# Optimization experiments

Measured on AMD Instinct MI355X. Metric: run time of the kernel, lower is better.

Reference implementation:

```python
import jax, jax.numpy as jnp
import numpy as np

D = 4  # downsample factor

def _conv1x1(x, w, b):
    # x: [B,C,H,W], w: [O,C], b: [O]
    return jnp.einsum('bchw,oc->bohw', x, w) + b[None, :, None, None]

def _maxpool(y):
    B, c, h, w = y.shape
    return y.reshape(B, c, h // D, D, w // D, D).max(axis=(3, 5))

def setup_inputs() -> dict:
    key = jax.random.key(0)
    ks = jax.random.split(key, 8)
    B, C, H, W = 4, 128, 256, 256
    cqk = C // 8
    s = 0.05
    return {
        'x':  jax.random.normal(ks[0], (B, C, H, W), jnp.float32),
        'wq': jax.random.normal(ks[1], (cqk, C), jnp.float32) * s,
        'bq': jnp.zeros((cqk,), jnp.float32),
        'wk': jax.random.normal(ks[2], (cqk, C), jnp.float32) * s,
        'bk': jnp.zeros((cqk,), jnp.float32),
        'wv': jax.random.normal(ks[3], (C, C), jnp.float32) * s,
        'bv': jnp.zeros((C,), jnp.float32),
        'gamma': jnp.zeros((1,), jnp.float32),
    }

def reference(x, wq, bq, wk, bk, wv, bv, gamma):
    B, C, H, W = x.shape
    N = (H // D) * (W // D)
    q = _maxpool(_conv1x1(x, wq, bq)).reshape(B, -1, N).transpose(0, 2, 1)  # [B,N,c]
    k = _maxpool(_conv1x1(x, wk, bk)).reshape(B, -1, N)                     # [B,c,N]
    energy = jnp.einsum('bnc,bcm->bnm', q, k)                               # [B,N,N]
    attention = jax.nn.softmax(energy, axis=-1)
    v = _maxpool(_conv1x1(x, wv, bv)).reshape(B, C, N)                      # [B,C,N]
    # torch: matmul(v, attention^T) -> out[b,c,m] = sum_n v[b,c,n] * attn[b,m,n]
    out = jnp.einsum('bcn,bmn->bcm', v, attention)
    out = out.reshape(B, C, H // D, W // D)
    out = jnp.repeat(jnp.repeat(out, D, axis=2), D, axis=3)  # nearest upsample
    out = gamma * out + x
    return out, attention
```

## Files before the change

### kernel.cpp

```cpp
#include <hip/hip_runtime.h>

#define B_ 4
#define C_ 128
#define H_ 256
#define W_ 256
#define CQK 16
#define NPOOL 4096
#define KSPLIT 2

typedef short bf16x8 __attribute__((ext_vector_type(8)));
typedef float f32x4 __attribute__((ext_vector_type(4)));
typedef float f32x2 __attribute__((ext_vector_type(2)));
typedef unsigned short ushort8 __attribute__((ext_vector_type(8)));

__device__ __forceinline__ unsigned short f2bf(float f) {
    unsigned int u = __float_as_uint(f);
    unsigned int r = (u + 0x7fffu + ((u >> 16) & 1u)) >> 16;
    return (unsigned short)r;
}

__global__ __launch_bounds__(256) void qk_conv_k(
    const float* __restrict__ x,
    const float* __restrict__ wq, const float* __restrict__ bq,
    const float* __restrict__ wk, const float* __restrict__ bk,
    const float* __restrict__ gamma,
    float* __restrict__ qpT, float* __restrict__ kp,
    float* __restrict__ out)
{
    if (gamma[0] != 0.0f) return;

    const int wh = blockIdx.x;
    const int ph = blockIdx.y;
    const int b  = blockIdx.z;
    const int t  = threadIdx.x;
    const int hl = t >> 6;
    const int ln = t & 63;

    __shared__ float wlds[C_ * 36];
    __shared__ float red[4 * 32 * 33];

    #pragma unroll
    for (int q = 0; q < 16; ++q) {
        const int idx = q*256 + t;
        const int c = idx & 127, o = idx >> 7;
        wlds[c*36 + o] = (o < 16) ? wq[o*C_ + c] : wk[(o-16)*C_ + c];
    }
    __syncthreads();

    float acc[32][2];
    #pragma unroll
    for (int o = 0; o < 32; ++o) { acc[o][0] = 0.f; acc[o][1] = 0.f; }

    const size_t base = ((size_t)(b*C_)*H_ + ph*4 + hl)*W_ + wh*128 + ln*2;
    const f32x2* xp = (const f32x2*)(x + base);
    f32x2*       op = (f32x2*)(out + base);

    f32x2 pre[4];
    #pragma unroll
    for (int q = 0; q < 4; ++q) pre[q] = xp[(size_t)q * 32768];

    #pragma unroll 4
    for (int c = 0; c < C_; ++c) {
        const f32x2 xv = pre[c & 3];
        if (c + 4 < C_) pre[c & 3] = xp[(size_t)(c + 4) * 32768];
        __builtin_nontemporal_store(xv, &op[(size_t)c * 32768]);
        const float* wrow = &wlds[c*36];
        #pragma unroll
        for (int og = 0; og < 8; ++og) {
            const f32x4 w4 = *(const f32x4*)&wrow[og*4];
            #pragma unroll
            for (int j = 0; j < 4; ++j) {
                acc[og*4+j][0] = fmaf(w4[j], xv[0], acc[og*4+j][0]);
                acc[og*4+j][1] = fmaf(w4[j], xv[1], acc[og*4+j][1]);
            }
        }
    }

    #pragma unroll
    for (int o = 0; o < 32; ++o) {
        float mm = fmaxf(acc[o][0], acc[o][1]);
        mm = fmaxf(mm, __shfl_xor(mm, 1));
        if (!(ln & 1)) red[(hl*32 + (ln >> 1))*33 + o] = mm;
    }
    __syncthreads();

    const int n0 = ph*64 + wh*32;
    #pragma unroll
    for (int q = 0; q < 4; ++q) {
        const int p = q*256 + t;
        const int o = p & 31, j = p >> 5;
        float val = fmaxf(fmaxf(red[(0*32+j)*33+o], red[(1*32+j)*33+o]),
                          fmaxf(red[(2*32+j)*33+o], red[(3*32+j)*33+o]));
        const int n = n0 + j;
        if (o < 16) { val += bq[o];    qpT[((size_t)b*NPOOL + n)*CQK + o] = val; }
        else        { val += bk[o-16]; kp[(b*CQK + (o-16))*NPOOL + n] = val; }
    }
}

__global__ __launch_bounds__(256) void qkv_pool_k(
    const float* __restrict__ x,
    const float* __restrict__ wq, const float* __restrict__ bq,
    const float* __restrict__ wk, const float* __restrict__ bk,
    const float* __restrict__ wv, const float* __restrict__ bv,
    const float* __restrict__ gamma,
    float* __restrict__ qpT, float* __restrict__ kp,
    unsigned short* __restrict__ vbf)
{
    if (gamma[0] == 0.0f) return;

    const int og = blockIdx.x;
    const int qw = blockIdx.y;
    const int b  = blockIdx.z >> 6;
    const int ph = blockIdx.z & 63;
    const int t  = threadIdx.x;
    const int o0 = og * 32;

    __shared__ float xs[32][256];
    __shared__ float wst[32][36];
    __shared__ float red[2][16][33];

    const int oq    = t & 7;
    const int tp    = t >> 3;
    const int hl_lo = tp >> 4;
    const int w4    = tp & 15;

    float acc[2][4][4];
    #pragma unroll
    for (int a = 0; a < 2; ++a)
        #pragma unroll
        for (int j = 0; j < 4; ++j)
            #pragma unroll
            for (int k = 0; k < 4; ++k) acc[a][j][k] = 0.f;

    const int hb = t >> 6;
    const int wb = t & 63;

    for (int c0 = 0; c0 < C_; c0 += 32) {
        __syncthreads();
        #pragma unroll 4
        for (int cl = 0; cl < 32; ++cl) {
            xs[cl][t] = x[((size_t)((b*C_ + c0 + cl)*H_ + ph*4 + hb))*W_ + qw*64 + wb];
        }
        {
            const int idx = t * 4;
            const int cl  = idx >> 5;
            const int olb = idx & 31;
            #pragma unroll
            for (int j = 0; j < 4; ++j) {
                const int ol = olb + j;
                const int o  = o0 + ol;
                const int c  = c0 + cl;
                float wv_;
                if (o < 16)      wv_ = wq[o*C_ + c];
                else if (o < 32) wv_ = wk[(o-16)*C_ + c];
                else             wv_ = wv[(o-32)*C_ + c];
                wst[cl][ol] = wv_;
            }
        }
        __syncthreads();
        for (int cl = 0; cl < 32; ++cl) {
            const float4 wv4 = *(const float4*)&wst[cl][oq*4];
            const float4 xa  = *(const float4*)&xs[cl][hl_lo*64 + w4*4];
            const float4 xb  = *(const float4*)&xs[cl][(2+hl_lo)*64 + w4*4];
            const float wr[4]  = {wv4.x, wv4.y, wv4.z, wv4.w};
            const float xar[4] = {xa.x, xa.y, xa.z, xa.w};
            const float xbr[4] = {xb.x, xb.y, xb.z, xb.w};
            #pragma unroll
            for (int j = 0; j < 4; ++j)
                #pragma unroll
                for (int k = 0; k < 4; ++k) {
                    acc[0][j][k] = fmaf(wr[j], xar[k], acc[0][j][k]);
                    acc[1][j][k] = fmaf(wr[j], xbr[k], acc[1][j][k]);
                }
        }
    }

    float m[4];
    #pragma unroll
    for (int j = 0; j < 4; ++j) {
        float mm = acc[0][j][0];
        #pragma unroll
        for (int k = 0; k < 4; ++k) {
            mm = fmaxf(mm, acc[0][j][k]);
            mm = fmaxf(mm, acc[1][j][k]);
        }
        m[j] = mm;
    }
    __syncthreads();
    #pragma unroll
    for (int j = 0; j < 4; ++j) red[hl_lo][w4][oq*4 + j] = m[j];
    __syncthreads();

    const int n0 = ph*64 + qw*16;
    #pragma unroll
    for (int r = 0; r < 2; ++r) {
        const int ii = t + r*256;
        const int pw = ii & 15, o = ii >> 4;
        float val = fmaxf(red[0][pw][o], red[1][pw][o]);
        const int n = n0 + pw;
        if (og == 0) {
            if (o < 16) { val += bq[o];    qpT[((size_t)b*NPOOL + n)*CQK + o] = val; }
            else        { val += bk[o-16]; kp[(b*CQK + (o-16))*NPOOL + n] = val; }
        } else {
            const int c = o0 - 32 + o;
            val += bv[c];
            vbf[(size_t)(b*C_ + c)*NPOOL + n] = f2bf(val);
        }
    }
}

__global__ __launch_bounds__(256) void attn_k(
    const float* __restrict__ qpT, const float* __restrict__ kp,
    float* __restrict__ attn)
{
    const int bid = blockIdx.x;
    const int b  = bid >> 10;
    const int i0 = (bid & 1023) * 4;
    const int t  = threadIdx.x;

    __shared__ float qs[4][16];
    __shared__ float wredm[4][4];
    __shared__ float wreds[4][4];

    if (t < 64) {
        const int i = t >> 4, c = t & 15;
        qs[i][c] = qpT[((size_t)b*NPOOL + i0 + i)*CQK + c];
    }
    __syncthreads();

    float acc[4][16];
    #pragma unroll
    for (int i = 0; i < 4; ++i)
        #pragma unroll
        for (int j = 0; j < 16; ++j) acc[i][j] = 0.f;

    const f32x4* k4 = (const f32x4*)kp;
    for (int c = 0; c < CQK; ++c) {
        float qr[4];
        #pragma unroll
        for (int i = 0; i < 4; ++i) qr[i] = qs[i][c];
        #pragma unroll
        for (int u = 0; u < 4; ++u) {
            const f32x4 kv = k4[(((size_t)(b*CQK + c))*NPOOL >> 2) + u*256 + t];
            #pragma unroll
            for (int i = 0; i < 4; ++i)
                #pragma unroll
                for (int e = 0; e < 4; ++e)
                    acc[i][u*4+e] = fmaf(qr[i], kv[e], acc[i][u*4+e]);
        }
    }

    const int wid = t >> 6, lane = t & 63;

    float rmax[4];
    #pragma unroll
    for (int i = 0; i < 4; ++i) {
        float lm = acc[i][0];
        #pragma unroll
        for (int j = 1; j < 16; ++j) lm = fmaxf(lm, acc[i][j]);
        #pragma unroll
        for (int off = 32; off; off >>= 1) lm = fmaxf(lm, __shfl_xor(lm, off));
        if (lane == 0) wredm[i][wid] = lm;
    }
    __syncthreads();
    #pragma unroll
    for (int i = 0; i < 4; ++i)
        rmax[i] = fmaxf(fmaxf(wredm[i][0], wredm[i][1]), fmaxf(wredm[i][2], wredm[i][3]));

    #pragma unroll
    for (int i = 0; i < 4; ++i) {
        float ls = 0.f;
        #pragma unroll
        for (int j = 0; j < 16; ++j) { acc[i][j] = __expf(acc[i][j] - rmax[i]); ls += acc[i][j]; }
        #pragma unroll
        for (int off = 32; off; off >>= 1) ls += __shfl_xor(ls, off);
        if (lane == 0) wreds[i][wid] = ls;
    }
    __syncthreads();
    f32x4* a4 = (f32x4*)attn;
    #pragma unroll
    for (int i = 0; i < 4; ++i) {
        const float s   = wreds[i][0] + wreds[i][1] + wreds[i][2] + wreds[i][3];
        const float inv = 1.0f / s;
        const size_t base = ((size_t)(b*NPOOL + i0 + i) * NPOOL) >> 2;
        #pragma unroll
        for (int u = 0; u < 4; ++u) {
            f32x4 r;
            r[0] = acc[i][u*4+0]*inv; r[1] = acc[i][u*4+1]*inv;
            r[2] = acc[i][u*4+2]*inv; r[3] = acc[i][u*4+3]*inv;
            __builtin_nontemporal_store(r, &a4[base + u*256 + t]);
        }
    }
}

__global__ __launch_bounds__(256) void pv_mfma_k(
    const unsigned short* __restrict__ vb, const float* __restrict__ attn,
    const float* __restrict__ gamma, float* __restrict__ os)
{
    if (gamma[0] == 0.0f) return;

    const int it = blockIdx.x;
    const int b  = blockIdx.y;
    const int z  = blockIdx.z;
    const int i0 = it * 128;
    const int t  = threadIdx.x;
    const int lane = t & 63, wid = t >> 6;
    const int wm = wid >> 1, wn = wid & 1;
    const int lr = lane & 15, lg = lane >> 4;

    __shared__ unsigned short As[128 * 72];
    __shared__ unsigned short Bs[128 * 72];

    f32x4 acc[4][4];
    #pragma unroll
    for (int m = 0; m < 4; ++m)
        #pragma unroll
        for (int n = 0; n < 4; ++n)
            acc[m][n] = (f32x4){0.f, 0.f, 0.f, 0.f};

    const int rowA = t >> 3;
    const int cb   = (t & 7) * 8;

    ushort8 ra[4];
    float4  rb[4][2];

    auto load_tile = [&](int nn) {
        #pragma unroll
        for (int p = 0; p < 4; ++p) {
            const int r = p * 32 + rowA;
            ra[p] = *(const ushort8*)&vb[(size_t)(b*C_ + r)*NPOOL + nn + cb];
            const float* src = &attn[(size_t)(b*NPOOL + i0 + r)*NPOOL + nn + cb];
            rb[p][0] = *(const float4*)src;
            rb[p][1] = *(const float4*)(src + 4);
        }
    };

    int nn = z * (NPOOL / KSPLIT);
    load_tile(nn);

    for (int s = 0; s < (NPOOL / KSPLIT) / 64; ++s) {
        __syncthreads();
        #pragma unroll
        for (int p = 0; p < 4; ++p) {
            const int r = p * 32 + rowA;
            *(ushort8*)&As[r*72 + cb] = ra[p];
            ushort8 ub;
            ub[0] = f2bf(rb[p][0].x); ub[1] = f2bf(rb[p][0].y);
            ub[2] = f2bf(rb[p][0].z); ub[3] = f2bf(rb[p][0].w);
            ub[4] = f2bf(rb[p][1].x); ub[5] = f2bf(rb[p][1].y);
            ub[6] = f2bf(rb[p][1].z); ub[7] = f2bf(rb[p][1].w);
            *(ushort8*)&Bs[r*72 + cb] = ub;
        }
        __syncthreads();
        if (s < (NPOOL / KSPLIT) / 64 - 1) load_tile(nn + 64);
        nn += 64;

        #pragma unroll
        for (int kk = 0; kk < 2; ++kk) {
            bf16x8 af[4], bq[4];
            #pragma unroll
            for (int m = 0; m < 4; ++m)
                af[m] = *(const bf16x8*)&As[(wm*64 + m*16 + lr)*72 + kk*32 + lg*8];
            #pragma unroll
            for (int n = 0; n < 4; ++n)
                bq[n] = *(const bf16x8*)&Bs[(wn*64 + n*16 + lr)*72 + kk*32 + lg*8];
            #pragma unroll
            for (int m = 0; m < 4; ++m)
                #pragma unroll
                for (int n = 0; n < 4; ++n)
                    acc[m][n] = __builtin_amdgcn_mfma_f32_16x16x32_bf16(
                        af[m], bq[n], acc[m][n], 0, 0, 0);
        }
    }

    #pragma unroll
    for (int m = 0; m < 4; ++m)
        #pragma unroll
        for (int n = 0; n < 4; ++n) {
            const int c0r = wm*64 + m*16 + lg*4;
            const int ig  = i0 + wn*64 + n*16 + lr;
            #pragma unroll
            for (int j = 0; j < 4; ++j)
                os[((size_t)((z*B_ + b)*C_ + c0r + j))*NPOOL + ig] = acc[m][n][j];
        }
}

__global__ __launch_bounds__(256) void up_res_k(
    const float* __restrict__ os, const float* __restrict__ x,
    const float* __restrict__ gamma, float* __restrict__ out)
{
    const float g = gamma[0];
    if (g == 0.0f) return;

    const int idx = blockIdx.x * 256 + threadIdx.x;
    const int w4 = idx & 63;
    const int h  = (idx >> 6) & 255;
    const int bc = idx >> 14;
    const float4 xv = *(const float4*)&x[(size_t)idx * 4];
    const size_t sidx = ((size_t)bc*64 + (h >> 2))*64 + w4;
    const size_t OSS  = (size_t)B_*C_*NPOOL;
    const float ov = os[sidx] + os[OSS + sidx];
    float4 r;
    r.x = g*ov + xv.x; r.y = g*ov + xv.y; r.z = g*ov + xv.z; r.w = g*ov + xv.w;
    *(float4*)&out[(size_t)idx * 4] = r;
}

extern "C" void kernel_launch(void* const* d_in, const int* in_sizes, int n_in,
                              void* d_out, int out_size, void* d_ws, size_t ws_size,
                              hipStream_t stream)
{
    const float* x     = (const float*)d_in[0];
    const float* wq    = (const float*)d_in[1];
    const float* bq    = (const float*)d_in[2];
    const float* wk    = (const float*)d_in[3];
    const float* bk    = (const float*)d_in[4];
    const float* wv    = (const float*)d_in[5];
    const float* bv    = (const float*)d_in[6];
    const float* gamma = (const float*)d_in[7];

    float* out  = (float*)d_out;
    float* attn = out + (size_t)B_*C_*H_*W_;

    float*          qpT = (float*)d_ws;
    float*          kp  = qpT + (size_t)B_*CQK*NPOOL;
    unsigned short* vbf = (unsigned short*)(kp + (size_t)B_*CQK*NPOOL);
    float*          os  = (float*)((char*)d_ws + (size_t)6*1024*1024);

    qk_conv_k<<<dim3(2, 64, B_), 256, 0, stream>>>(x, wq, bq, wk, bk, gamma,
                                                   qpT, kp, out);
    qkv_pool_k<<<dim3(5, 4, B_*64), 256, 0, stream>>>(x, wq, bq, wk, bk, wv, bv,
                                                      gamma, qpT, kp, vbf);
    attn_k<<<B_*1024, 256, 0, stream>>>(qpT, kp, attn);
    pv_mfma_k<<<dim3(NPOOL/128, B_, KSPLIT), 256, 0, stream>>>(vbf, attn, gamma, os);
    up_res_k<<<(B_*C_*H_*W_/4)/256, 256, 0, stream>>>(os, x, gamma, out);
}
```

Before: 228.1 us.

## Widen conv blocks to full rows with float4 loads and enlarge attention row tiles

The gamma==0 Q/K conv kernel now gives each block a full 256-wide strip of four rows. Each thread loads float4 and keeps packed f32x2 accumulators, so pooling within a 4-wide window happens in registers instead of via a shuffle. The attention kernel now handles 8 query rows per 512-thread block instead of 4 rows per 256 threads, which halves redundant K reads per output row and halves the block count. The risks are higher register pressure from the doubled per-thread accumulators and fewer conv blocks (256) to fill the GPU.

```diff
diff --git a/kernel.cpp b/kernel.cpp
--- a/kernel.cpp
+++ b/kernel.cpp
@@ -19,7 +19,7 @@
     return (unsigned short)r;
 }
 
-__global__ __launch_bounds__(256) void qk_conv_k(
+__global__ __launch_bounds__(256) void qk_conv2_k(
     const float* __restrict__ x,
     const float* __restrict__ wq, const float* __restrict__ bq,
     const float* __restrict__ wk, const float* __restrict__ bk,
@@ -29,69 +29,72 @@
 {
     if (gamma[0] != 0.0f) return;
 
-    const int wh = blockIdx.x;
-    const int ph = blockIdx.y;
-    const int b  = blockIdx.z;
+    const int bx = blockIdx.x;
+    const int b  = blockIdx.y;
     const int t  = threadIdx.x;
     const int hl = t >> 6;
     const int ln = t & 63;
 
-    __shared__ float wlds[C_ * 36];
-    __shared__ float red[4 * 32 * 33];
+    __shared__ float wlds[C_ * 32];
+    __shared__ float red[4][64][33];
 
     #pragma unroll
     for (int q = 0; q < 16; ++q) {
         const int idx = q*256 + t;
-        const int c = idx & 127, o = idx >> 7;
-        wlds[c*36 + o] = (o < 16) ? wq[o*C_ + c] : wk[(o-16)*C_ + c];
-    }
-    __syncthreads();
-
-    float acc[32][2];
-    #pragma unroll
-    for (int o = 0; o < 32; ++o) { acc[o][0] = 0.f; acc[o][1] = 0.f; }
-
-    const size_t base = ((size_t)(b*C_)*H_ + ph*4 + hl)*W_ + wh*128 + ln*2;
-    const f32x2* xp = (const f32x2*)(x + base);
-    f32x2*       op = (f32x2*)(out + base);
-
-    f32x2 pre[4];
-    #pragma unroll
-    for (int q = 0; q < 4; ++q) pre[q] = xp[(size_t)q * 32768];
+        const int c = idx >> 5, o = idx & 31;
+        wlds[idx] = (o < 16) ? wq[o*C_ + c] : wk[(o-16)*C_ + c];
+    }
+    __syncthreads();
+
+    f32x2 acc[32][2];
+    #pragma unroll
+    for (int o = 0; o < 32; ++o) {
+        acc[o][0] = (f32x2){0.f, 0.f};
+        acc[o][1] = (f32x2){0.f, 0.f};
+    }
+
+    const size_t base4 = ((size_t)(b*C_)*H_ + bx*4 + hl)*(W_/4) + ln;
+    const f32x4* xp = (const f32x4*)x;
+    f32x4*       op = (f32x4*)out;
+
+    f32x4 pre[4];
+    #pragma unroll
+    for (int q = 0; q < 4; ++q) pre[q] = xp[base4 + (size_t)q*16384];
 
     #pragma unroll 4
     for (int c = 0; c < C_; ++c) {
-        const f32x2 xv = pre[c & 3];
-        if (c + 4 < C_) pre[c & 3] = xp[(size_t)(c + 4) * 32768];
-        __builtin_nontemporal_store(xv, &op[(size_t)c * 32768]);
-        const float* wrow = &wlds[c*36];
+        const f32x4 v = pre[c & 3];
+        if (c + 4 < C_) pre[c & 3] = xp[base4 + (size_t)(c + 4)*16384];
+        __builtin_nontemporal_store(v, &op[base4 + (size_t)c*16384]);
+        const f32x2 xa = (f32x2){v[0], v[1]};
+        const f32x2 xb = (f32x2){v[2], v[3]};
+        const float* wrow = &wlds[c*32];
         #pragma unroll
         for (int og = 0; og < 8; ++og) {
             const f32x4 w4 = *(const f32x4*)&wrow[og*4];
             #pragma unroll
             for (int j = 0; j < 4; ++j) {
-                acc[og*4+j][0] = fmaf(w4[j], xv[0], acc[og*4+j][0]);
-                acc[og*4+j][1] = fmaf(w4[j], xv[1], acc[og*4+j][1]);
+                const f32x2 ws = (f32x2){w4[j], w4[j]};
+                acc[og*4+j][0] += ws * xa;
+                acc[og*4+j][1] += ws * xb;
             }
         }
     }
 
     #pragma unroll
     for (int o = 0; o < 32; ++o) {
-        float mm = fmaxf(acc[o][0], acc[o][1]);
-        mm = fmaxf(mm, __shfl_xor(mm, 1));
-        if (!(ln & 1)) red[(hl*32 + (ln >> 1))*33 + o] = mm;
-    }
-    __syncthreads();
-
-    const int n0 = ph*64 + wh*32;
-    #pragma unroll
-    for (int q = 0; q < 4; ++q) {
-        const int p = q*256 + t;
-        const int o = p & 31, j = p >> 5;
-        float val = fmaxf(fmaxf(red[(0*32+j)*33+o], red[(1*32+j)*33+o]),
-                          fmaxf(red[(2*32+j)*33+o], red[(3*32+j)*33+o]));
-        const int n = n0 + j;
+        red[hl][ln][o] = fmaxf(fmaxf(acc[o][0][0], acc[o][0][1]),
+                               fmaxf(acc[o][1][0], acc[o][1][1]));
+    }
+    __syncthreads();
+
+    #pragma unroll
+    for (int q = 0; q < 8; ++q) {
+        const int idx = q*256 + t;
+        const int o = idx & 31, pc = (idx >> 5) & 63;
+        float val = fmaxf(fmaxf(red[0][pc][o], red[1][pc][o]),
+                          fmaxf(red[2][pc][o], red[3][pc][o]));
+        const int n = bx*64 + pc;
         if (o < 16) { val += bq[o];    qpT[((size_t)b*NPOOL + n)*CQK + o] = val; }
         else        { val += bk[o-16]; kp[(b*CQK + (o-16))*NPOOL + n] = val; }
     }
@@ -209,86 +212,94 @@
     }
 }
 
-__global__ __launch_bounds__(256) void attn_k(
+__global__ __launch_bounds__(512) void attn8_k(
     const float* __restrict__ qpT, const float* __restrict__ kp,
     float* __restrict__ attn)
 {
-    const int bid = blockIdx.x;
-    const int b  = bid >> 10;
-    const int i0 = (bid & 1023) * 4;
+    const int it = blockIdx.x;
+    const int b  = blockIdx.y;
+    const int i0 = it * 8;
     const int t  = threadIdx.x;
 
-    __shared__ float qs[4][16];
-    __shared__ float wredm[4][4];
-    __shared__ float wreds[4][4];
-
-    if (t < 64) {
+    __shared__ float qs[8][16];
+    __shared__ float wredm[8][8];
+    __shared__ float wreds[8][8];
+
+    if (t < 128) {
         const int i = t >> 4, c = t & 15;
         qs[i][c] = qpT[((size_t)b*NPOOL + i0 + i)*CQK + c];
     }
     __syncthreads();
 
-    float acc[4][16];
-    #pragma unroll
-    for (int i = 0; i < 4; ++i)
-        #pragma unroll
-        for (int j = 0; j < 16; ++j) acc[i][j] = 0.f;
+    float acc[8][8];
+    #pragma unroll
+    for (int i = 0; i < 8; ++i)
+        #pragma unroll
+        for (int j = 0; j < 8; ++j) acc[i][j] = 0.f;
 
     const f32x4* k4 = (const f32x4*)kp;
     for (int c = 0; c < CQK; ++c) {
-        float qr[4];
-        #pragma unroll
-        for (int i = 0; i < 4; ++i) qr[i] = qs[i][c];
-        #pragma unroll
-        for (int u = 0; u < 4; ++u) {
-            const f32x4 kv = k4[(((size_t)(b*CQK + c))*NPOOL >> 2) + u*256 + t];
-            #pragma unroll
-            for (int i = 0; i < 4; ++i)
-                #pragma unroll
-                for (int e = 0; e < 4; ++e)
-                    acc[i][u*4+e] = fmaf(qr[i], kv[e], acc[i][u*4+e]);
-        }
-    }
-
-    const int wid = t >> 6, lane = t & 63;
-
-    float rmax[4];
-    #pragma unroll
-    for (int i = 0; i < 4; ++i) {
+        const size_t kb = ((size_t)(b*CQK + c))*NPOOL >> 2;
+        const f32x4 kv0 = k4[kb + t];
+        const f32x4 kv1 = k4[kb + 512 + t];
+        float qr[8];
+        #pragma unroll
+        for (int i = 0; i < 8; ++i) qr[i] = qs[i][c];
+        #pragma unroll
+        for (int i = 0; i < 8; ++i)
+            #pragma unroll
+            for (int e = 0; e < 4; ++e) {
+                acc[i][e]   = fmaf(qr[i], kv0[e], acc[i][e]);
+                acc[i][4+e] = fmaf(qr[i], kv1[e], acc[i][4+e]);
+            }
+    }
+
+    const int wv = t >> 6, lane = t & 63;
+
+    float rmax[8];
+    #pragma unroll
+    for (int i = 0; i < 8; ++i) {
         float lm = acc[i][0];
         #pragma unroll
-        for (int j = 1; j < 16; ++j) lm = fmaxf(lm, acc[i][j]);
+        for (int j = 1; j < 8; ++j) lm = fmaxf(lm, acc[i][j]);
         #pragma unroll
         for (int off = 32; off; off >>= 1) lm = fmaxf(lm, __shfl_xor(lm, off));
-        if (lane == 0) wredm[i][wid] = lm;
-    }
-    __syncthreads();
-    #pragma unroll
-    for (int i = 0; i < 4; ++i)
-        rmax[i] = fmaxf(fmaxf(wredm[i][0], wredm[i][1]), fmaxf(wredm[i][2], wredm[i][3]));
-
-    #pragma unroll
-    for (int i = 0; i < 4; ++i) {
+        if (lane == 0) wredm[i][wv] = lm;
+    }
+    __syncthreads();
+    #pragma unroll
+    for (int i = 0; i < 8; ++i) {
+        float m = wredm[i][0];
+        #pragma unroll
+        for (int w8 = 1; w8 < 8; ++w8) m = fmaxf(m, wredm[i][w8]);
+        rmax[i] = m;
+    }
+
+    #pragma unroll
+    for (int i = 0; i < 8; ++i) {
         float ls = 0.f;
         #pragma unroll
-        for (int j = 0; j < 16; ++j) { acc[i][j] = __expf(acc[i][j] - rmax[i]); ls += acc[i][j]; }
+        for (int j = 0; j < 8; ++j) { acc[i][j] = __expf(acc[i][j] - rmax[i]); ls += acc[i][j]; }
         #pragma unroll
         for (int off = 32; off; off >>= 1) ls += __shfl_xor(ls, off);
-        if (lane == 0) wreds[i][wid] = ls;
-    }
-    __syncthreads();
+        if (lane == 0) wreds[i][wv] = ls;
+    }
+    __syncthreads();
+
     f32x4* a4 = (f32x4*)attn;
     #pragma unroll
-    for (int i = 0; i < 4; ++i) {
-        const float s   = wreds[i][0] + wreds[i][1] + wreds[i][2] + wreds[i][3];
+    for (int i = 0; i < 8; ++i) {
+        float s = wreds[i][0];
+        #pragma unroll
+        for (int w8 = 1; w8 < 8; ++w8) s += wreds[i][w8];
         const float inv = 1.0f / s;
         const size_t base = ((size_t)(b*NPOOL + i0 + i) * NPOOL) >> 2;
         #pragma unroll
-        for (int u = 0; u < 4; ++u) {
+        for (int u = 0; u < 2; ++u) {
             f32x4 r;
             r[0] = acc[i][u*4+0]*inv; r[1] = acc[i][u*4+1]*inv;
             r[2] = acc[i][u*4+2]*inv; r[3] = acc[i][u*4+3]*inv;
-            __builtin_nontemporal_store(r, &a4[base + u*256 + t]);
+            __builtin_nontemporal_store(r, &a4[base + u*512 + t]);
         }
     }
 }
@@ -426,11 +437,11 @@
     unsigned short* vbf = (unsigned short*)(kp + (size_t)B_*CQK*NPOOL);
     float*          os  = (float*)((char*)d_ws + (size_t)6*1024*1024);
 
-    qk_conv_k<<<dim3(2, 64, B_), 256, 0, stream>>>(x, wq, bq, wk, bk, gamma,
-                                                   qpT, kp, out);
+    qk_conv2_k<<<dim3(64, B_), 256, 0, stream>>>(x, wq, bq, wk, bk, gamma,
+                                                 qpT, kp, out);
     qkv_pool_k<<<dim3(5, 4, B_*64), 256, 0, stream>>>(x, wq, bq, wk, bk, wv, bv,
                                                       gamma, qpT, kp, vbf);
-    attn_k<<<B_*1024, 256, 0, stream>>>(qpT, kp, attn);
+    attn8_k<<<dim3(NPOOL/8, B_), 512, 0, stream>>>(qpT, kp, attn);
     pv_mfma_k<<<dim3(NPOOL/128, B_, KSPLIT), 256, 0, stream>>>(vbf, attn, gamma, os);
     up_res_k<<<(B_*C_*H_*W_/4)/256, 256, 0, stream>>>(os, x, gamma, out);
 }
```

After: 188.1 us. -17.6%, faster.
